# Kernel optimization log

Measured on AMD Instinct MI355X. Metric: run time of the kernel, lower is better.

The kernel has to match this reference:

```python
import jax, jax.numpy as jnp
import numpy as np

ALPHA = 0.2  # LeakyReLU negative slope
NEG_BIG = jnp.float32(-9e15)


def _leaky_relu(x):
    return jnp.where(x > 0, x, ALPHA * x)


def gat_layer(h, adj, w, a):
    """One GATLayer with concat=True (ELU output), dropout=0 (eval mode).
    h: [N, F_in], adj: [N, N] int, w: [F_in, F_out], a: [2*F_out, 1].
    """
    Wh = h @ w                         # [N, F_out]
    f_out = w.shape[1]
    Wh1 = Wh @ a[:f_out]               # [N, 1]
    Wh2 = Wh @ a[f_out:]               # [N, 1]
    e = _leaky_relu(Wh1 + Wh2.T)       # [N, N] dense additive scores
    att = jnp.where(adj > 0, e, NEG_BIG)
    att = jax.nn.softmax(att, axis=1)  # row softmax
    return jax.nn.elu(att @ Wh)        # [N, F_out]


def setup_inputs() -> dict:
    N, F_IN, H, NHEADS = 4096, 128, 64, 4
    key = jax.random.key(0)
    ks = jax.random.split(key, 9)
    s = jnp.float32(0.1)  # keep logits in a sane range
    x = jax.random.normal(ks[0], (N, F_IN), jnp.float32)
    adj = jax.random.randint(ks[1], (N, N), 0, 2, jnp.int32)
    return {
        "x": x,
        "adj": adj,
        "w_heads": jax.random.normal(ks[2], (NHEADS, F_IN, H), jnp.float32) * s,
        "a_heads": jax.random.normal(ks[3], (NHEADS, 2 * H, 1), jnp.float32) * s,
        "w_out": jax.random.normal(ks[4], (NHEADS * H, H), jnp.float32) * s,
        "a_out": jax.random.normal(ks[5], (2 * H, 1), jnp.float32) * s,
        "lin_w": jax.random.normal(ks[6], (H, F_IN), jnp.float32) * s,
        "lin_b": jnp.zeros((H,), jnp.float32),
        "outlin_w": jax.random.normal(ks[7], (H, H), jnp.float32) * s,
        "outlin_b": jnp.zeros((H,), jnp.float32),
    }


def reference(x, adj, w_heads, a_heads, w_out, a_out, lin_w, lin_b, outlin_w, outlin_b):
    N = x.shape[0]
    x_residual = x @ lin_w.T + lin_b                      # nn.Linear(input, hidden)
    # multi-head GAT layers, concatenated along features
    heads = jax.vmap(gat_layer, in_axes=(None, None, 0, 0))(x, adj, w_heads, a_heads)  # [nh, N, H]
    hcat = jnp.transpose(heads, (1, 0, 2)).reshape(N, -1)  # [N, nh*H]
    out = gat_layer(hcat, adj, w_out, a_out)               # out_att (concat=True => ELU)
    out = (x_residual + out) @ outlin_w.T + outlin_b       # out_linear
    return jax.nn.elu(out)
```

## Files before the change

### kernel.cpp

```cpp
#include <hip/hip_runtime.h>
#include <hip/hip_bf16.h>
#include <stdint.h>

#define F_IN 128
#define H 64
#define NH 4
#define KCH_H 4
#define KCH_O 16
#define LOG2E 1.44269504088896f

typedef __attribute__((ext_vector_type(8))) short bf16x8;
typedef __attribute__((ext_vector_type(4))) float floatx4;

__global__ void pack_adjp_kernel(const int* __restrict__ adj,
                                 unsigned char* __restrict__ adjp, int N) {
    size_t gid = (size_t)blockIdx.x * 256 + threadIdx.x;
    int v = adj[gid];
    unsigned long long m = __ballot(v > 0);
    int lane = threadIdx.x & 63;
    if ((lane & 7) == 0) {
        int b = lane >> 3;
        size_t row = gid / N;
        int j = (int)(gid - row * N);
        int kt = j >> 5, q = (j >> 3) & 3;
        int KT = N >> 5;
        adjp[((row >> 4) * (size_t)KT + kt) * 64 + q * 16 + (row & 15)] =
            (unsigned char)(m >> (b * 8));
    }
}

__global__ void wh_kernel(const float* __restrict__ x,
                          const float* __restrict__ w_heads,
                          float* __restrict__ Wh_all, int N) {
    int tid = threadIdx.x;
    int h = tid >> 6, f = tid & 63;
    int i0 = blockIdx.x * 8;
    __shared__ float xs[8][F_IN];
    for (int e = tid; e < 8 * F_IN; e += 256)
        xs[e >> 7][e & 127] = x[(size_t)(i0 + (e >> 7)) * F_IN + (e & 127)];
    __syncthreads();
    float acc[8];
#pragma unroll
    for (int r = 0; r < 8; ++r) acc[r] = 0.f;
    const float* w = w_heads + (size_t)h * F_IN * H + f;
#pragma unroll 4
    for (int k = 0; k < F_IN; ++k) {
        float wv = w[(size_t)k * H];
#pragma unroll
        for (int r = 0; r < 8; ++r) acc[r] += xs[r][k] * wv;
    }
#pragma unroll
    for (int r = 0; r < 8; ++r)
        Wh_all[((size_t)h * N + i0 + r) * H + f] = acc[r];
}

__global__ void xres_kernel(const float* __restrict__ x,
                            const float* __restrict__ lin_w,
                            const float* __restrict__ lin_b,
                            float* __restrict__ x_res, int N) {
    int tid = threadIdx.x;
    int f = tid & 63, rl = tid >> 6;
    int i0 = blockIdx.x * 8;
    __shared__ float xs[8][F_IN];
    for (int e = tid; e < 8 * F_IN; e += 256)
        xs[e >> 7][e & 127] = x[(size_t)(i0 + (e >> 7)) * F_IN + (e & 127)];
    __syncthreads();
    float a0 = 0.f, a1 = 0.f;
#pragma unroll 4
    for (int k = 0; k < F_IN; ++k) {
        float wv = lin_w[(size_t)f * F_IN + k];
        a0 += xs[rl][k] * wv;
        a1 += xs[rl + 4][k] * wv;
    }
    float b = lin_b[f];
    x_res[(size_t)(i0 + rl) * H + f] = a0 + b;
    x_res[(size_t)(i0 + rl + 4) * H + f] = a1 + b;
}

__global__ void scores_kernel(const float* __restrict__ Wh,
                              const float* __restrict__ a,
                              float* __restrict__ s1, float* __restrict__ s2,
                              int N, int nh) {
    int idx = blockIdx.x * blockDim.x + threadIdx.x;
    if (idx >= nh * N) return;
    int h = idx / N, i = idx - h * N;
    const float* row = Wh + ((size_t)h * N + i) * H;
    const float* a1 = a + (size_t)h * 2 * H;
    const float* a2 = a1 + H;
    float acc1 = 0.f, acc2 = 0.f;
#pragma unroll 8
    for (int f = 0; f < H; ++f) {
        float v = row[f];
        acc1 += v * a1[f];
        acc2 += v * a2[f];
    }
    s1[(size_t)h * N + i] = acc1 * LOG2E;
    s2[(size_t)h * N + i] = acc2 * LOG2E;
}

__global__ void bpack_kernel(const float* __restrict__ src,
                             unsigned short* __restrict__ dst, int N) {
    int h = blockIdx.y, kt = blockIdx.x;
    int KT = N >> 5;
    int tid = threadIdx.x;
    int g = tid >> 6, lane = tid & 63;
    int q = lane >> 4, n = lane & 15;
    const float* s = src + ((size_t)h * N + kt * 32 + q * 8) * 64 + g * 16 + n;
    unsigned short tmp[8];
#pragma unroll
    for (int jj = 0; jj < 8; ++jj) {
        __hip_bfloat16 b = __float2bfloat16(s[(size_t)jj * 64]);
        tmp[jj] = *(unsigned short*)&b;
    }
    unsigned short* d = dst + (((size_t)(h * KT + kt) * 4 + g) * 64 + lane) * 8;
#pragma unroll
    for (int jj = 0; jj < 8; ++jj) d[jj] = tmp[jj];
}

template <int KTC>
__global__ __launch_bounds__(256, 4)
void pv2_kernel(const unsigned char* __restrict__ adjp,
                const unsigned short* __restrict__ Bpk,
                const float* __restrict__ s1a,
                const float* __restrict__ s2a,
                float* __restrict__ outp, float* __restrict__ lp,
                int out_stride, int N) {
    const int h = blockIdx.y, z = blockIdx.z;
    const int KT = N >> 5;
    const int kt0 = z * KTC;
    const int tid = threadIdx.x;
    const int wave = tid >> 6, lane = tid & 63;
    const int n = lane & 15, q = lane >> 4;
    const int i0w = (blockIdx.x * 4 + wave) * 16;

    __shared__ float s2s[KTC * 32];
    __shared__ unsigned short ldsB[2][2048];

    const float4* s2src = (const float4*)(s2a + (size_t)h * N + kt0 * 32);
    for (int e = tid; e < KTC * 8; e += 256) ((float4*)s2s)[e] = s2src[e];

    const unsigned short* Bb = Bpk + ((size_t)h * KT + kt0) * 2048;
    *(uint4*)&ldsB[0][tid * 8] = *(const uint4*)(Bb + tid * 8);

    const unsigned char* ap = adjp + ((size_t)(i0w >> 4) * KT + kt0) * 64 + lane;
    unsigned int a_c = ap[0];
    const float s1v = s1a[(size_t)h * N + i0w + n];

    floatx4 acc[4];
    floatx4 accl = {0.f, 0.f, 0.f, 0.f};
#pragma unroll
    for (int g = 0; g < 4; ++g) acc[g] = (floatx4){0.f, 0.f, 0.f, 0.f};

    bf16x8 ones;
    {
        short one = (n == 0) ? (short)0x3F80 : (short)0;
#pragma unroll
        for (int jj = 0; jj < 8; ++jj) ones[jj] = one;
    }

    __syncthreads();

#pragma unroll 2
    for (int k = 0; k < KTC; ++k) {
        const int cur = k & 1;
        const int kn = (k + 1 < KTC) ? k + 1 : k;
        uint4 bst = *(const uint4*)(Bb + (size_t)kn * 2048 + tid * 8);
        unsigned int a_n = ap[(size_t)kn * 64];

        float4 sa = *(const float4*)&s2s[k * 32 + q * 8];
        float4 sb = *(const float4*)&s2s[k * 32 + q * 8 + 4];
        const float* sv = (const float*)&sa;
        const float* sw = (const float*)&sb;
        float e[8];
#pragma unroll
        for (int jj = 0; jj < 8; ++jj) {
            float sj = (jj < 4 ? sv[jj] : sw[jj - 4]);
            float tt = s1v + sj;
            float lr = fmaxf(tt, 0.2f * tt);
            lr = (a_c & (1u << jj)) ? lr : -150.f;
            e[jj] = __builtin_amdgcn_exp2f(lr);
        }
        union { unsigned int u[4]; bf16x8 v; } u;
        u.u[0] = __builtin_amdgcn_perm(__float_as_uint(e[1]), __float_as_uint(e[0]), 0x07060302u);
        u.u[1] = __builtin_amdgcn_perm(__float_as_uint(e[3]), __float_as_uint(e[2]), 0x07060302u);
        u.u[2] = __builtin_amdgcn_perm(__float_as_uint(e[5]), __float_as_uint(e[4]), 0x07060302u);
        u.u[3] = __builtin_amdgcn_perm(__float_as_uint(e[7]), __float_as_uint(e[6]), 0x07060302u);

        bf16x8 bf0 = *(const bf16x8*)&ldsB[cur][0 * 512 + lane * 8];
        bf16x8 bf1 = *(const bf16x8*)&ldsB[cur][1 * 512 + lane * 8];
        bf16x8 bf2 = *(const bf16x8*)&ldsB[cur][2 * 512 + lane * 8];
        bf16x8 bf3 = *(const bf16x8*)&ldsB[cur][3 * 512 + lane * 8];

        acc[0] = __builtin_amdgcn_mfma_f32_16x16x32_bf16(u.v, bf0, acc[0], 0, 0, 0);
        acc[1] = __builtin_amdgcn_mfma_f32_16x16x32_bf16(u.v, bf1, acc[1], 0, 0, 0);
        acc[2] = __builtin_amdgcn_mfma_f32_16x16x32_bf16(u.v, bf2, acc[2], 0, 0, 0);
        acc[3] = __builtin_amdgcn_mfma_f32_16x16x32_bf16(u.v, bf3, acc[3], 0, 0, 0);
        accl   = __builtin_amdgcn_mfma_f32_16x16x32_bf16(u.v, ones, accl, 0, 0, 0);

        *(uint4*)&ldsB[cur ^ 1][tid * 8] = bst;
        a_c = a_n;
        __syncthreads();
    }

    float* obase = outp + ((size_t)z * N + i0w) * out_stride + h * 64;
#pragma unroll
    for (int r = 0; r < 4; ++r) {
        int rr = q * 4 + r;
        float* op = obase + (size_t)rr * out_stride + n;
        op[0]  = acc[0][r];
        op[16] = acc[1][r];
        op[32] = acc[2][r];
        op[48] = acc[3][r];
    }
    if (n == 0) {
        float* lrow = lp + ((size_t)z * gridDim.y + h) * N + i0w;
#pragma unroll
        for (int r = 0; r < 4; ++r) lrow[q * 4 + r] = accl[r];
    }
}

__global__ void whout2_kernel(const float* __restrict__ hcp,
                              const float* __restrict__ lhp,
                              const float* __restrict__ w_out,
                              float* __restrict__ Wh_out, int N) {
    int tid = threadIdx.x;
    int i0 = blockIdx.x * 8;
    __shared__ float hs[8][256];
    __shared__ float linv[8][NH];
    if (tid < 8 * NH) {
        int r = tid >> 2, hd = tid & 3;
        float l = 0.f;
#pragma unroll
        for (int p = 0; p < KCH_H; ++p)
            l += lhp[((size_t)p * NH + hd) * N + i0 + r];
        linv[r][hd] = 1.f / fmaxf(l, 1e-30f);
    }
    __syncthreads();
    const size_t ps = (size_t)N * 256;
    for (int e = tid; e < 8 * 256; e += 256) {
        int r = e >> 8, k = e & 255;
        size_t off = (size_t)(i0 + r) * 256 + k;
        float v = hcp[off] + hcp[ps + off] + hcp[2 * ps + off] + hcp[3 * ps + off];
        v *= linv[r][k >> 6];
        hs[r][k] = v > 0.f ? v : expm1f(v);
    }
    __syncthreads();
    int f = tid & 63, rl = tid >> 6;
    float a0 = 0.f, a1 = 0.f;
#pragma unroll 4
    for (int k = 0; k < 256; ++k) {
        float wv = w_out[(size_t)k * H + f];
        a0 += hs[rl][k] * wv;
        a1 += hs[rl + 4][k] * wv;
    }
    Wh_out[(size_t)(i0 + rl) * H + f] = a0;
    Wh_out[(size_t)(i0 + rl + 4) * H + f] = a1;
}

__global__ void final2_kernel(const float* __restrict__ o2p,
                              const float* __restrict__ lop,
                              const float* __restrict__ x_res,
                              const float* __restrict__ outlin_w,
                              const float* __restrict__ outlin_b,
                              float* __restrict__ out, int N) {
    int tid = threadIdx.x;
    int f = tid & 63, rl = tid >> 6;
    int i0 = blockIdx.x * 8;
    __shared__ float hs[8][H];
    __shared__ float linv[8];
    if (tid < 8) {
        float l = 0.f;
#pragma unroll
        for (int p = 0; p < KCH_O; ++p) l += lop[(size_t)p * N + i0 + tid];
        linv[tid] = 1.f / fmaxf(l, 1e-30f);
    }
    __syncthreads();
    const size_t ps = (size_t)N * 64;
    for (int e = tid; e < 8 * 64; e += 256) {
        int r = e >> 6, ff = e & 63;
        size_t off = (size_t)(i0 + r) * 64 + ff;
        float v = 0.f;
#pragma unroll
        for (int p = 0; p < KCH_O; ++p) v += o2p[p * ps + off];
        v *= linv[r];
        v = v > 0.f ? v : expm1f(v);
        hs[r][ff] = v + x_res[off];
    }
    __syncthreads();
    float b = outlin_b[f];
    float a0 = b, a1 = b;
#pragma unroll 8
    for (int k = 0; k < H; ++k) {
        float wv = outlin_w[(size_t)f * H + k];
        a0 += hs[rl][k] * wv;
        a1 += hs[rl + 4][k] * wv;
    }
    a0 = a0 > 0.f ? a0 : expm1f(a0);
    a1 = a1 > 0.f ? a1 : expm1f(a1);
    out[(size_t)(i0 + rl) * H + f] = a0;
    out[(size_t)(i0 + rl + 4) * H + f] = a1;
}

extern "C" void kernel_launch(void* const* d_in, const int* in_sizes, int n_in,
                              void* d_out, int out_size, void* d_ws, size_t ws_size,
                              hipStream_t stream) {
    const float* x        = (const float*)d_in[0];
    const int*   adj      = (const int*)d_in[1];
    const float* w_heads  = (const float*)d_in[2];
    const float* a_heads  = (const float*)d_in[3];
    const float* w_out    = (const float*)d_in[4];
    const float* a_out    = (const float*)d_in[5];
    const float* lin_w    = (const float*)d_in[6];
    const float* lin_b    = (const float*)d_in[7];
    const float* outlin_w = (const float*)d_in[8];
    const float* outlin_b = (const float*)d_in[9];
    float* out = (float*)d_out;

    const int N = in_sizes[0] / F_IN;
    const int KT = N >> 5;

    char* p = (char*)d_ws;
    float* part   = (float*)p;  p += (size_t)KCH_H * N * 256 * 4;
    float* Wh_all = (float*)p;  p += (size_t)NH * N * 64 * 4;
    float* x_res  = (float*)p;  p += (size_t)N * 64 * 4;
    float* Wh_out = (float*)p;  p += (size_t)N * 64 * 4;
    float* s1h    = (float*)p;  p += (size_t)NH * N * 4;
    float* s2h    = (float*)p;  p += (size_t)NH * N * 4;
    float* s1o    = (float*)p;  p += (size_t)N * 4;
    float* s2o    = (float*)p;  p += (size_t)N * 4;
    float* lh_part = (float*)p; p += (size_t)KCH_H * NH * N * 4;
    float* lo_part = (float*)p; p += (size_t)KCH_O * N * 4;
    unsigned short* Bpk  = (unsigned short*)p;  p += (size_t)NH * KT * 2048 * 2;
    unsigned short* BpkO = (unsigned short*)p;  p += (size_t)KT * 2048 * 2;
    unsigned char* adjp  = (unsigned char*)p;   p += (size_t)(N / 16) * KT * 64;

    pack_adjp_kernel<<<(size_t)N * N / 256, 256, 0, stream>>>(adj, adjp, N);
    wh_kernel<<<N / 8, 256, 0, stream>>>(x, w_heads, Wh_all, N);
    xres_kernel<<<N / 8, 256, 0, stream>>>(x, lin_w, lin_b, x_res, N);
    scores_kernel<<<(NH * N + 255) / 256, 256, 0, stream>>>(Wh_all, a_heads, s1h, s2h, N, NH);
    bpack_kernel<<<dim3(KT, NH), 256, 0, stream>>>(Wh_all, Bpk, N);

    pv2_kernel<32><<<dim3(N / 64, NH, KCH_H), 256, 0, stream>>>(
        adjp, Bpk, s1h, s2h, part, lh_part, NH * H, N);
    whout2_kernel<<<N / 8, 256, 0, stream>>>(part, lh_part, w_out, Wh_out, N);

    scores_kernel<<<(N + 255) / 256, 256, 0, stream>>>(Wh_out, a_out, s1o, s2o, N, 1);
    bpack_kernel<<<dim3(KT, 1), 256, 0, stream>>>(Wh_out, BpkO, N);
    pv2_kernel<8><<<dim3(N / 64, 1, KCH_O), 256, 0, stream>>>(
        adjp, BpkO, s1o, s2o, part, lo_part, H, N);
    final2_kernel<<<N / 8, 256, 0, stream>>>(part, lo_part, x_res, outlin_w, outlin_b, out, N);
}
```

Before: 235.7 us.

## Fuse projection, residual and score kernels; vectorize adjacency packing; raise split-K

```diff
diff --git a/kernel.cpp b/kernel.cpp
--- a/kernel.cpp
+++ b/kernel.cpp
@@ -5,33 +5,39 @@
 #define F_IN 128
 #define H 64
 #define NH 4
-#define KCH_H 4
+#define KCH_H 8
 #define KCH_O 16
 #define LOG2E 1.44269504088896f
 
 typedef __attribute__((ext_vector_type(8))) short bf16x8;
 typedef __attribute__((ext_vector_type(4))) float floatx4;
 
-__global__ void pack_adjp_kernel(const int* __restrict__ adj,
-                                 unsigned char* __restrict__ adjp, int N) {
-    size_t gid = (size_t)blockIdx.x * 256 + threadIdx.x;
-    int v = adj[gid];
-    unsigned long long m = __ballot(v > 0);
-    int lane = threadIdx.x & 63;
-    if ((lane & 7) == 0) {
-        int b = lane >> 3;
-        size_t row = gid / N;
-        int j = (int)(gid - row * N);
-        int kt = j >> 5, q = (j >> 3) & 3;
-        int KT = N >> 5;
-        adjp[((row >> 4) * (size_t)KT + kt) * 64 + q * 16 + (row & 15)] =
-            (unsigned char)(m >> (b * 8));
-    }
-}
-
-__global__ void wh_kernel(const float* __restrict__ x,
-                          const float* __restrict__ w_heads,
-                          float* __restrict__ Wh_all, int N) {
+__global__ void pack_adjp_kernel(const int4* __restrict__ adj4,
+                                 unsigned char* __restrict__ adjp,
+                                 int N, int KT) {
+    int row = blockIdx.y;
+    int c0 = (blockIdx.x * 256 + threadIdx.x) * 8;
+    const int4* p = adj4 + ((size_t)row * N + c0) / 4;
+    int4 a = p[0], b = p[1];
+    unsigned int byte =
+        (unsigned)(a.x > 0) | ((unsigned)(a.y > 0) << 1) |
+        ((unsigned)(a.z > 0) << 2) | ((unsigned)(a.w > 0) << 3) |
+        ((unsigned)(b.x > 0) << 4) | ((unsigned)(b.y > 0) << 5) |
+        ((unsigned)(b.z > 0) << 6) | ((unsigned)(b.w > 0) << 7);
+    int kt = c0 >> 5, q = (c0 >> 3) & 3;
+    adjp[((size_t)(row >> 4) * KT + kt) * 64 + q * 16 + (row & 15)] =
+        (unsigned char)byte;
+}
+
+__global__ void wh_fused_kernel(const float* __restrict__ x,
+                                const float* __restrict__ w_heads,
+                                const float* __restrict__ a_heads,
+                                const float* __restrict__ lin_w,
+                                const float* __restrict__ lin_b,
+                                float* __restrict__ Wh_all,
+                                float* __restrict__ x_res,
+                                float* __restrict__ s1h,
+                                float* __restrict__ s2h, int N) {
     int tid = threadIdx.x;
     int h = tid >> 6, f = tid & 63;
     int i0 = blockIdx.x * 8;
@@ -42,60 +48,40 @@
     float acc[8];
 #pragma unroll
     for (int r = 0; r < 8; ++r) acc[r] = 0.f;
+    float xr0 = 0.f, xr1 = 0.f;
     const float* w = w_heads + (size_t)h * F_IN * H + f;
+    const float* lw = lin_w + (size_t)f * F_IN;
 #pragma unroll 4
     for (int k = 0; k < F_IN; ++k) {
         float wv = w[(size_t)k * H];
 #pragma unroll
         for (int r = 0; r < 8; ++r) acc[r] += xs[r][k] * wv;
+        float wx = lw[k];
+        xr0 += xs[h][k] * wx;
+        xr1 += xs[h + 4][k] * wx;
     }
 #pragma unroll
     for (int r = 0; r < 8; ++r)
         Wh_all[((size_t)h * N + i0 + r) * H + f] = acc[r];
-}
-
-__global__ void xres_kernel(const float* __restrict__ x,
-                            const float* __restrict__ lin_w,
-                            const float* __restrict__ lin_b,
-                            float* __restrict__ x_res, int N) {
-    int tid = threadIdx.x;
-    int f = tid & 63, rl = tid >> 6;
-    int i0 = blockIdx.x * 8;
-    __shared__ float xs[8][F_IN];
-    for (int e = tid; e < 8 * F_IN; e += 256)
-        xs[e >> 7][e & 127] = x[(size_t)(i0 + (e >> 7)) * F_IN + (e & 127)];
-    __syncthreads();
-    float a0 = 0.f, a1 = 0.f;
-#pragma unroll 4
-    for (int k = 0; k < F_IN; ++k) {
-        float wv = lin_w[(size_t)f * F_IN + k];
-        a0 += xs[rl][k] * wv;
-        a1 += xs[rl + 4][k] * wv;
-    }
     float b = lin_b[f];
-    x_res[(size_t)(i0 + rl) * H + f] = a0 + b;
-    x_res[(size_t)(i0 + rl + 4) * H + f] = a1 + b;
-}
-
-__global__ void scores_kernel(const float* __restrict__ Wh,
-                              const float* __restrict__ a,
-                              float* __restrict__ s1, float* __restrict__ s2,
-                              int N, int nh) {
-    int idx = blockIdx.x * blockDim.x + threadIdx.x;
-    if (idx >= nh * N) return;
-    int h = idx / N, i = idx - h * N;
-    const float* row = Wh + ((size_t)h * N + i) * H;
-    const float* a1 = a + (size_t)h * 2 * H;
-    const float* a2 = a1 + H;
-    float acc1 = 0.f, acc2 = 0.f;
-#pragma unroll 8
-    for (int f = 0; f < H; ++f) {
-        float v = row[f];
-        acc1 += v * a1[f];
-        acc2 += v * a2[f];
-    }
-    s1[(size_t)h * N + i] = acc1 * LOG2E;
-    s2[(size_t)h * N + i] = acc2 * LOG2E;
+    x_res[(size_t)(i0 + h) * H + f] = xr0 + b;
+    x_res[(size_t)(i0 + h + 4) * H + f] = xr1 + b;
+    float a1v = a_heads[(size_t)h * 2 * H + f];
+    float a2v = a_heads[(size_t)h * 2 * H + H + f];
+#pragma unroll
+    for (int r = 0; r < 8; ++r) {
+        float t1 = acc[r] * a1v;
+        float t2 = acc[r] * a2v;
+#pragma unroll
+        for (int off = 32; off > 0; off >>= 1) {
+            t1 += __shfl_xor(t1, off, 64);
+            t2 += __shfl_xor(t2, off, 64);
+        }
+        if (f == 0) {
+            s1h[(size_t)h * N + i0 + r] = t1 * LOG2E;
+            s2h[(size_t)h * N + i0 + r] = t2 * LOG2E;
+        }
+    }
 }
 
 __global__ void bpack_kernel(const float* __restrict__ src,
@@ -118,7 +104,7 @@
 }
 
 template <int KTC>
-__global__ __launch_bounds__(256, 4)
+__global__ __launch_bounds__(256, 8)
 void pv2_kernel(const unsigned char* __restrict__ adjp,
                 const unsigned short* __restrict__ Bpk,
                 const float* __restrict__ s1a,
@@ -222,7 +208,10 @@
 __global__ void whout2_kernel(const float* __restrict__ hcp,
                               const float* __restrict__ lhp,
                               const float* __restrict__ w_out,
-                              float* __restrict__ Wh_out, int N) {
+                              const float* __restrict__ a_out,
+                              float* __restrict__ Wh_out,
+                              float* __restrict__ s1o,
+                              float* __restrict__ s2o, int N) {
     int tid = threadIdx.x;
     int i0 = blockIdx.x * 8;
     __shared__ float hs[8][256];
@@ -240,7 +229,9 @@
     for (int e = tid; e < 8 * 256; e += 256) {
         int r = e >> 8, k = e & 255;
         size_t off = (size_t)(i0 + r) * 256 + k;
-        float v = hcp[off] + hcp[ps + off] + hcp[2 * ps + off] + hcp[3 * ps + off];
+        float v = 0.f;
+#pragma unroll
+        for (int p = 0; p < KCH_H; ++p) v += hcp[p * ps + off];
         v *= linv[r][k >> 6];
         hs[r][k] = v > 0.f ? v : expm1f(v);
     }
@@ -255,6 +246,21 @@
     }
     Wh_out[(size_t)(i0 + rl) * H + f] = a0;
     Wh_out[(size_t)(i0 + rl + 4) * H + f] = a1;
+    float w1 = a_out[f], w2 = a_out[H + f];
+    float t10 = a0 * w1, t20 = a0 * w2, t11 = a1 * w1, t21 = a1 * w2;
+#pragma unroll
+    for (int off = 32; off > 0; off >>= 1) {
+        t10 += __shfl_xor(t10, off, 64);
+        t20 += __shfl_xor(t20, off, 64);
+        t11 += __shfl_xor(t11, off, 64);
+        t21 += __shfl_xor(t21, off, 64);
+    }
+    if (f == 0) {
+        s1o[i0 + rl] = t10 * LOG2E;
+        s2o[i0 + rl] = t20 * LOG2E;
+        s1o[i0 + rl + 4] = t11 * LOG2E;
+        s2o[i0 + rl + 4] = t21 * LOG2E;
+    }
 }
 
 __global__ void final2_kernel(const float* __restrict__ o2p,
@@ -334,17 +340,15 @@
     unsigned short* BpkO = (unsigned short*)p;  p += (size_t)KT * 2048 * 2;
     unsigned char* adjp  = (unsigned char*)p;   p += (size_t)(N / 16) * KT * 64;
 
-    pack_adjp_kernel<<<(size_t)N * N / 256, 256, 0, stream>>>(adj, adjp, N);
-    wh_kernel<<<N / 8, 256, 0, stream>>>(x, w_heads, Wh_all, N);
-    xres_kernel<<<N / 8, 256, 0, stream>>>(x, lin_w, lin_b, x_res, N);
-    scores_kernel<<<(NH * N + 255) / 256, 256, 0, stream>>>(Wh_all, a_heads, s1h, s2h, N, NH);
+    pack_adjp_kernel<<<dim3(N / 2048, N), 256, 0, stream>>>((const int4*)adj, adjp, N, KT);
+    wh_fused_kernel<<<N / 8, 256, 0, stream>>>(x, w_heads, a_heads, lin_w, lin_b,
+                                               Wh_all, x_res, s1h, s2h, N);
     bpack_kernel<<<dim3(KT, NH), 256, 0, stream>>>(Wh_all, Bpk, N);
 
-    pv2_kernel<32><<<dim3(N / 64, NH, KCH_H), 256, 0, stream>>>(
+    pv2_kernel<16><<<dim3(N / 64, NH, KCH_H), 256, 0, stream>>>(
         adjp, Bpk, s1h, s2h, part, lh_part, NH * H, N);
-    whout2_kernel<<<N / 8, 256, 0, stream>>>(part, lh_part, w_out, Wh_out, N);
-
-    scores_kernel<<<(N + 255) / 256, 256, 0, stream>>>(Wh_out, a_out, s1o, s2o, N, 1);
+    whout2_kernel<<<N / 8, 256, 0, stream>>>(part, lh_part, w_out, a_out,
+                                             Wh_out, s1o, s2o, N);
     bpack_kernel<<<dim3(KT, 1), 256, 0, stream>>>(Wh_out, BpkO, N);
     pv2_kernel<8><<<dim3(N / 64, 1, KCH_O), 256, 0, stream>>>(
         adjp, BpkO, s1o, s2o, part, lo_part, H, N);
```

New measurement: 206.0 us. 1.14x faster.
